# Performance work log

Measured on AMD Instinct MI355X. Metric: run time of the kernel, lower is better.

The kernel has to match this reference:

```python
import math
import jax, jax.numpy as jnp
import numpy as np

B, S, D, H = 4, 2048, 1024, 16
DH = D // H  # 64


def setup_inputs() -> dict:
    key = jax.random.key(0)
    k1, k2, k3 = jax.random.split(key, 3)
    x = jax.random.normal(k1, (B, S, D), dtype=jnp.float32)
    W_qkv = jax.random.normal(k2, (D, 3 * D), dtype=jnp.float32) * (1.0 / math.sqrt(D))
    b_qkv = jax.random.normal(k3, (3 * D,), dtype=jnp.float32) * 0.02
    return {"x": x, "W_qkv": W_qkv, "b_qkv": b_qkv}


def reference(x, W_qkv, b_qkv):
    b, s, d = x.shape
    qkv = x @ W_qkv + b_qkv                       # [B,S,3D]
    # Faithful to torch: view(B,S,H,3,D_h) -> interleaved per-head q/k/v split
    qkv = qkv.reshape(b, s, H, 3, DH)
    q = jnp.transpose(qkv[:, :, :, 0, :], (0, 2, 1, 3))  # [B,H,S,DH]
    k = jnp.transpose(qkv[:, :, :, 1, :], (0, 2, 1, 3))
    v = jnp.transpose(qkv[:, :, :, 2, :], (0, 2, 1, 3))
    scores = jnp.einsum('bhsd,bhtd->bhst', q, k) / math.sqrt(DH)  # [B,H,S,S]
    causal = jnp.triu(jnp.ones((s, s), dtype=bool), k=1)
    scores = jnp.where(causal, -jnp.inf, scores)
    weights = jax.nn.softmax(scores, axis=-1)
    # dropout is identity in eval/reference mode
    context = jnp.einsum('bhst,bhtd->bhsd', weights, v)  # [B,H,S,DH]
    return jnp.transpose(context, (0, 2, 1, 3)).reshape(b, s, d)
```

## Files before the change

### kernel.cpp

```cpp
#include <hip/hip_runtime.h>
#include <hip/hip_bf16.h>

#define Bz 4
#define Sz 2048
#define Dz 1024
#define Hz 16
#define DHz 64
#define Mz (Bz*Sz)
#define N3z (3*Dz)
#define Kz Dz

typedef short s16x8 __attribute__((ext_vector_type(8)));
typedef float f32x4 __attribute__((ext_vector_type(4)));
typedef unsigned short u16;

__device__ __forceinline__ u16 f2b(float f) {
  union { float f; unsigned u; } v; v.f = f;
  unsigned r = v.u + 0x7FFFu + ((v.u >> 16) & 1u);
  return (u16)(r >> 16);
}

__device__ __forceinline__ unsigned cvt_pk_bf16(float lo, float hi) {
  unsigned r;
  asm("v_cvt_pk_bf16_f32 %0, %1, %2" : "=v"(r) : "v"(lo), "v"(hi));
  return r;
}

__global__ __launch_bounds__(256) void cvt_x(const float* __restrict__ x,
                                             u16* __restrict__ xb) {
  int i = (blockIdx.x * 256 + threadIdx.x) * 4;
  float4 v = *reinterpret_cast<const float4*>(x + i);
  ushort4 o;
  o.x = f2b(v.x); o.y = f2b(v.y); o.z = f2b(v.z); o.w = f2b(v.w);
  *reinterpret_cast<ushort4*>(xb + i) = o;
}

__global__ __launch_bounds__(256) void transpose_w(const float* __restrict__ W,
                                                   u16* __restrict__ Wt) {
  __shared__ u16 t[32][33];
  int nb = blockIdx.x;
  int kb = blockIdx.y;
  int tx = threadIdx.x, ty = threadIdx.y;
#pragma unroll
  for (int j = 0; j < 4; ++j) {
    int k = kb * 32 + ty + j * 8;
    t[ty + j * 8][tx] = f2b(W[(size_t)k * N3z + nb * 32 + tx]);
  }
  __syncthreads();
#pragma unroll
  for (int j = 0; j < 4; ++j) {
    int n = nb * 32 + ty + j * 8;
    Wt[(size_t)n * Kz + kb * 32 + tx] = t[tx][ty + j * 8];
  }
}

#define BM 128
#define BN 128
#define BKs 32
#define QSCALE (0.125f * 1.44269504088896f)

__global__ __launch_bounds__(256) void qkv_gemm(
    const u16* __restrict__ A, const u16* __restrict__ Bt,
    const float* __restrict__ bias,
    u16* __restrict__ Qo, u16* __restrict__ Ko, u16* __restrict__ Vo) {
  __shared__ alignas(16) u16 As[BM * BKs];
  __shared__ alignas(16) u16 Bs[BN * BKs];
  const int tid = threadIdx.x;
  const int wid = tid >> 6, lane = tid & 63;
  const int wr = wid >> 1, wc = wid & 1;
  const int g = lane >> 4, lq = lane & 15;
  const int brow = blockIdx.x * BM;
  const int bcol = blockIdx.y * BN;

  f32x4 acc[4][4] = {};

  for (int kt = 0; kt < Kz; kt += BKs) {
#pragma unroll
    for (int c = 0; c < 2; ++c) {
      int row = (wid * 2 + c) * 16 + (lane >> 2);
      int off = (lane & 3) * 8;
      const u16* ga = A + (size_t)(brow + row) * Kz + kt + off;
      __builtin_amdgcn_global_load_lds(
          (const __attribute__((address_space(1))) void*)ga,
          (__attribute__((address_space(3))) void*)&As[(wid * 2 + c) * 512],
          16, 0, 0);
      const u16* gb = Bt + (size_t)(bcol + row) * Kz + kt + off;
      __builtin_amdgcn_global_load_lds(
          (const __attribute__((address_space(1))) void*)gb,
          (__attribute__((address_space(3))) void*)&Bs[(wid * 2 + c) * 512],
          16, 0, 0);
    }
    __syncthreads();

    s16x8 af[4], bfr[4];
#pragma unroll
    for (int i = 0; i < 4; ++i) {
      af[i]  = *reinterpret_cast<const s16x8*>(&As[(wr * 64 + i * 16 + lq) * BKs + g * 8]);
      bfr[i] = *reinterpret_cast<const s16x8*>(&Bs[(wc * 64 + i * 16 + lq) * BKs + g * 8]);
    }
#pragma unroll
    for (int mi = 0; mi < 4; ++mi)
#pragma unroll
      for (int ni = 0; ni < 4; ++ni)
        acc[mi][ni] = __builtin_amdgcn_mfma_f32_16x16x32_bf16(af[mi], bfr[ni], acc[mi][ni], 0, 0, 0);
    __syncthreads();
  }

#pragma unroll
  for (int ni = 0; ni < 4; ++ni) {
    int gcol = bcol + wc * 64 + ni * 16 + lq;
    int h = gcol / 192;
    int rem = gcol - h * 192;
    int tt = rem >> 6;
    int dh = rem & 63;
    float bv = bias[gcol];
    u16* dst = (tt == 0) ? Qo : (tt == 1) ? Ko : Vo;
    float scale = (tt == 0) ? QSCALE : 1.0f;
#pragma unroll
    for (int mi = 0; mi < 4; ++mi) {
#pragma unroll
      for (int r = 0; r < 4; ++r) {
        int grow = brow + wr * 64 + mi * 16 + g * 4 + r;
        int bb = grow >> 11;
        int ss = grow & 2047;
        float v = (acc[mi][ni][r] + bv) * scale;
        dst[(((size_t)bb * Hz + h) * Sz + ss) * DHz + dh] = f2b(v);
      }
    }
  }
}

__global__ __launch_bounds__(512, 4) void attn_kernel(
    const u16* __restrict__ Qg, const u16* __restrict__ Kg,
    const u16* __restrict__ Vg, float* __restrict__ out) {
  __shared__ alignas(16) u16 Ks[64 * 64];
  __shared__ alignas(16) u16 Vs[64 * 64];

  const int qpair = blockIdx.x;
  const int bh = blockIdx.y;
  const int tid = threadIdx.x;
  const int wid = tid >> 6, lane = tid & 63;
  const int g = lane >> 4, lq = lane & 15;
  const size_t base = (size_t)bh * Sz * DHz;
  const int b = bh >> 4, h = bh & 15;

  const int krow = tid >> 3;
  const int kslot = tid & 7;
  const int kswz = kslot ^ (krow & 7);
  const int vkey = tid & 63;
  const int vdh0 = (tid >> 6) * 8;

  char* KsB = (char*)Ks;
  char* VsB = (char*)Vs;

  const int p = g & 1;
  const int cb = g >> 1;
  const int sA = 32 * (g & 1) + lq;
  const int sB = sA + 16;
  const int sEven = cb ? sB : sA;
  const int sOdd  = cb ? sA : sB;

  for (int half = 0; half < 2; ++half) {
    const int qt = half ? (15 - qpair) : qpair;
    const int q0w = qt * 128 + wid * 16;
    const int qrow = q0w + lq;

    s16x8 qf0 = *reinterpret_cast<const s16x8*>(Qg + base + (size_t)(q0w + lq) * DHz + g * 8);
    s16x8 qf1 = *reinterpret_cast<const s16x8*>(Qg + base + (size_t)(q0w + lq) * DHz + g * 8 + 32);

    f32x4 o[4] = {};
    float m1 = -1e30f;
    float l1 = 0.f;

    const int nt = 2 * qt + 2;
    for (int t = 0; t < nt; ++t) {
      const int kv0 = t * 64;

      s16x8 kvv = *reinterpret_cast<const s16x8*>(Kg + base + (size_t)(kv0 + krow) * DHz + kslot * 8);
      *reinterpret_cast<s16x8*>(KsB + krow * 128 + kswz * 16) = kvv;
      s16x8 vvv = *reinterpret_cast<const s16x8*>(Vg + base + (size_t)(kv0 + vkey) * DHz + vdh0);
#pragma unroll
      for (int j = 0; j < 8; ++j) {
        int byte = (vdh0 + j) * 128 + vkey * 2;
        byte ^= (j << 4);
        *reinterpret_cast<u16*>(VsB + byte) = (u16)vvv[j];
      }
      __syncthreads();

      const bool active = (kv0 <= q0w + 15);
      if (active) {
        f32x4 z[4];
#pragma unroll
        for (int f = 0; f < 4; ++f) {
          int row = f * 16 + lq;
          s16x8 kb0 = *reinterpret_cast<const s16x8*>(KsB + row * 128 + ((g ^ (row & 7)) << 4));
          s16x8 kb1 = *reinterpret_cast<const s16x8*>(KsB + row * 128 + (((g + 4) ^ (row & 7)) << 4));
          f32x4 zz = {0.f, 0.f, 0.f, 0.f};
          zz = __builtin_amdgcn_mfma_f32_16x16x32_bf16(kb0, qf0, zz, 0, 0, 0);
          zz = __builtin_amdgcn_mfma_f32_16x16x32_bf16(kb1, qf1, zz, 0, 0, 0);
          z[f] = zz;
        }

        if (kv0 + 63 > q0w) {
#pragma unroll
          for (int f = 0; f < 4; ++f)
#pragma unroll
            for (int r = 0; r < 4; ++r) {
              int key = kv0 + f * 16 + g * 4 + r;
              if (key > qrow) z[f][r] = -1e30f;
            }
        }

        float pm = z[0][0];
#pragma unroll
        for (int f = 0; f < 4; ++f)
#pragma unroll
          for (int r = 0; r < 4; ++r) pm = fmaxf(pm, z[f][r]);
        pm = fmaxf(pm, __shfl_xor(pm, 16));
        pm = fmaxf(pm, __shfl_xor(pm, 32));

        if (!__all(pm <= m1 + 8.0f)) {
          float mn = fmaxf(m1, pm);
          float a = exp2f(m1 - mn);
          m1 = mn;
          l1 *= a;
          float a0 = __shfl(a, 4 * g + 0);
          float a1 = __shfl(a, 4 * g + 1);
          float a2 = __shfl(a, 4 * g + 2);
          float a3 = __shfl(a, 4 * g + 3);
#pragma unroll
          for (int ni = 0; ni < 4; ++ni) {
            o[ni][0] *= a0; o[ni][1] *= a1; o[ni][2] *= a2; o[ni][3] *= a3;
          }
        }

        float s = 0.f;
        unsigned w[4][2];
#pragma unroll
        for (int f = 0; f < 4; ++f) {
          float p0 = exp2f(z[f][0] - m1);
          float p1 = exp2f(z[f][1] - m1);
          float p2 = exp2f(z[f][2] - m1);
          float p3 = exp2f(z[f][3] - m1);
          s += (p0 + p1) + (p2 + p3);
          w[f][0] = cvt_pk_bf16(p0, p1);
          w[f][1] = cvt_pk_bf16(p2, p3);
        }
        s += __shfl_xor(s, 16);
        s += __shfl_xor(s, 32);
        l1 += s;

        int e0 = __shfl((int)(p ? w[1][0] : w[0][0]), sEven);
        int o0 = __shfl((int)(p ? w[0][0] : w[1][0]), sOdd);
        int e1 = __shfl((int)(p ? w[1][1] : w[0][1]), sEven);
        int o1 = __shfl((int)(p ? w[0][1] : w[1][1]), sOdd);
        int e2 = __shfl((int)(p ? w[3][0] : w[2][0]), sEven);
        int o2 = __shfl((int)(p ? w[2][0] : w[3][0]), sOdd);
        int e3 = __shfl((int)(p ? w[3][1] : w[2][1]), sEven);
        int o3 = __shfl((int)(p ? w[2][1] : w[3][1]), sOdd);
        union { int i[4]; s16x8 v; } A0, A1;
        A0.i[0] = cb ? o0 : e0;
        A0.i[2] = cb ? e0 : o0;
        A0.i[1] = cb ? o1 : e1;
        A0.i[3] = cb ? e1 : o1;
        A1.i[0] = cb ? o2 : e2;
        A1.i[2] = cb ? e2 : o2;
        A1.i[1] = cb ? o3 : e3;
        A1.i[3] = cb ? e3 : o3;

#pragma unroll
        for (int ni = 0; ni < 4; ++ni) {
          int row = ni * 16 + lq;
          s16x8 vb0 = *reinterpret_cast<const s16x8*>(VsB + row * 128 + ((g ^ (row & 7)) << 4));
          s16x8 vb1 = *reinterpret_cast<const s16x8*>(VsB + row * 128 + (((g + 4) ^ (row & 7)) << 4));
          o[ni] = __builtin_amdgcn_mfma_f32_16x16x32_bf16(A0.v, vb0, o[ni], 0, 0, 0);
          o[ni] = __builtin_amdgcn_mfma_f32_16x16x32_bf16(A1.v, vb1, o[ni], 0, 0, 0);
        }
      }
      __syncthreads();
    }

    float lr0 = __shfl(l1, 4 * g + 0);
    float lr1 = __shfl(l1, 4 * g + 1);
    float lr2 = __shfl(l1, 4 * g + 2);
    float lr3 = __shfl(l1, 4 * g + 3);
    float inv[4] = {1.0f / lr0, 1.0f / lr1, 1.0f / lr2, 1.0f / lr3};
#pragma unroll
    for (int r = 0; r < 4; ++r) {
      int s = q0w + g * 4 + r;
      float* op = out + (((size_t)b * Sz + s) * Hz + h) * DHz;
#pragma unroll
      for (int ni = 0; ni < 4; ++ni)
        op[ni * 16 + lq] = o[ni][r] * inv[r];
    }
  }
}

extern "C" void kernel_launch(void* const* d_in, const int* in_sizes, int n_in,
                              void* d_out, int out_size, void* d_ws, size_t ws_size,
                              hipStream_t stream) {
  const float* x    = (const float*)d_in[0];
  const float* W    = (const float*)d_in[1];
  const float* bias = (const float*)d_in[2];
  float* out = (float*)d_out;

  char* ws = (char*)d_ws;
  u16* xb = (u16*)(ws);
  u16* wt = (u16*)(ws + 16777216);
  u16* Qb = (u16*)(ws + 23068672);
  u16* Kb = (u16*)(ws + 39845888);
  u16* Vb = (u16*)(ws + 56623104);

  cvt_x<<<8192, 256, 0, stream>>>(x, xb);
  transpose_w<<<dim3(96, 32), dim3(32, 8), 0, stream>>>(W, wt);
  qkv_gemm<<<dim3(Mz / BM, N3z / BN), 256, 0, stream>>>(xb, wt, bias, Qb, Kb, Vb);
  attn_kernel<<<dim3(8, Bz * Hz), 512, 0, stream>>>(Qb, Kb, Vb, out);
}
```

Before: 233.5 us.

## Double-buffer K/V tiles in attention and widen GEMM K-tile with swizzled LDS

The attention kernel now keeps two LDS buffers for K and V. It prefetches the next tile into registers while the current one is being computed, then writes it to the other buffer, which removes one barrier per iteration and hides global load latency. The QKV GEMM moves to a 64-wide K tile with an XOR-swizzled LDS layout, halving the number of loop iterations and barriers and avoiding bank conflicts on fragment reads. In exchange, LDS use and register pressure go up, which may cut occupancy.

```diff
diff --git a/kernel.cpp b/kernel.cpp
--- a/kernel.cpp
+++ b/kernel.cpp
@@ -56,7 +56,7 @@
 
 #define BM 128
 #define BN 128
-#define BKs 32
+#define BKs 64
 #define QSCALE (0.125f * 1.44269504088896f)
 
 __global__ __launch_bounds__(256) void qkv_gemm(
@@ -72,37 +72,44 @@
   const int brow = blockIdx.x * BM;
   const int bcol = blockIdx.y * BN;
 
+  const int soff = (((lane & 7) ^ (lane >> 3))) * 8;
+
   f32x4 acc[4][4] = {};
 
   for (int kt = 0; kt < Kz; kt += BKs) {
 #pragma unroll
-    for (int c = 0; c < 2; ++c) {
-      int row = (wid * 2 + c) * 16 + (lane >> 2);
-      int off = (lane & 3) * 8;
-      const u16* ga = A + (size_t)(brow + row) * Kz + kt + off;
+    for (int c = 0; c < 4; ++c) {
+      int row = (wid * 4 + c) * 8 + (lane >> 3);
+      const u16* ga = A + (size_t)(brow + row) * Kz + kt + soff;
       __builtin_amdgcn_global_load_lds(
           (const __attribute__((address_space(1))) void*)ga,
-          (__attribute__((address_space(3))) void*)&As[(wid * 2 + c) * 512],
+          (__attribute__((address_space(3))) void*)&As[(wid * 4 + c) * 512],
           16, 0, 0);
-      const u16* gb = Bt + (size_t)(bcol + row) * Kz + kt + off;
+      const u16* gb = Bt + (size_t)(bcol + row) * Kz + kt + soff;
       __builtin_amdgcn_global_load_lds(
           (const __attribute__((address_space(1))) void*)gb,
-          (__attribute__((address_space(3))) void*)&Bs[(wid * 2 + c) * 512],
+          (__attribute__((address_space(3))) void*)&Bs[(wid * 4 + c) * 512],
           16, 0, 0);
     }
     __syncthreads();
 
-    s16x8 af[4], bfr[4];
-#pragma unroll
-    for (int i = 0; i < 4; ++i) {
-      af[i]  = *reinterpret_cast<const s16x8*>(&As[(wr * 64 + i * 16 + lq) * BKs + g * 8]);
-      bfr[i] = *reinterpret_cast<const s16x8*>(&Bs[(wc * 64 + i * 16 + lq) * BKs + g * 8]);
-    }
-#pragma unroll
-    for (int mi = 0; mi < 4; ++mi)
-#pragma unroll
-      for (int ni = 0; ni < 4; ++ni)
-        acc[mi][ni] = __builtin_amdgcn_mfma_f32_16x16x32_bf16(af[mi], bfr[ni], acc[mi][ni], 0, 0, 0);
+#pragma unroll
+    for (int ks = 0; ks < 2; ++ks) {
+      s16x8 af[4], bfr[4];
+#pragma unroll
+      for (int i = 0; i < 4; ++i) {
+        int rowa = wr * 64 + i * 16 + lq;
+        int rowb = wc * 64 + i * 16 + lq;
+        int sl = ((ks * 4 + g) ^ (lq & 7)) << 4;
+        af[i]  = *reinterpret_cast<const s16x8*>((const char*)As + rowa * 128 + sl);
+        bfr[i] = *reinterpret_cast<const s16x8*>((const char*)Bs + rowb * 128 + sl);
+      }
+#pragma unroll
+      for (int mi = 0; mi < 4; ++mi)
+#pragma unroll
+        for (int ni = 0; ni < 4; ++ni)
+          acc[mi][ni] = __builtin_amdgcn_mfma_f32_16x16x32_bf16(af[mi], bfr[ni], acc[mi][ni], 0, 0, 0);
+    }
     __syncthreads();
   }
 
@@ -133,8 +140,8 @@
 __global__ __launch_bounds__(512, 4) void attn_kernel(
     const u16* __restrict__ Qg, const u16* __restrict__ Kg,
     const u16* __restrict__ Vg, float* __restrict__ out) {
-  __shared__ alignas(16) u16 Ks[64 * 64];
-  __shared__ alignas(16) u16 Vs[64 * 64];
+  __shared__ alignas(16) u16 Ks[2][64 * 64];
+  __shared__ alignas(16) u16 Vs[2][64 * 64];
 
   const int qpair = blockIdx.x;
   const int bh = blockIdx.y;
@@ -150,9 +157,6 @@
   const int vkey = tid & 63;
   const int vdh0 = (tid >> 6) * 8;
 
-  char* KsB = (char*)Ks;
-  char* VsB = (char*)Vs;
-
   const int p = g & 1;
   const int cb = g >> 1;
   const int sA = 32 * (g & 1) + lq;
@@ -173,19 +177,33 @@
     float l1 = 0.f;
 
     const int nt = 2 * qt + 2;
+
+    {
+      s16x8 kc = *reinterpret_cast<const s16x8*>(Kg + base + (size_t)krow * DHz + kslot * 8);
+      s16x8 vc = *reinterpret_cast<const s16x8*>(Vg + base + (size_t)vkey * DHz + vdh0);
+      char* KB = (char*)Ks[0];
+      char* VB = (char*)Vs[0];
+      *reinterpret_cast<s16x8*>(KB + krow * 128 + kswz * 16) = kc;
+#pragma unroll
+      for (int j = 0; j < 8; ++j)
+        *reinterpret_cast<u16*>(VB + (((vdh0 + j) * 128 + vkey * 2) ^ (j << 4))) = (u16)vc[j];
+    }
+    __syncthreads();
+
+    int cur = 0;
     for (int t = 0; t < nt; ++t) {
       const int kv0 = t * 64;
-
-      s16x8 kvv = *reinterpret_cast<const s16x8*>(Kg + base + (size_t)(kv0 + krow) * DHz + kslot * 8);
-      *reinterpret_cast<s16x8*>(KsB + krow * 128 + kswz * 16) = kvv;
-      s16x8 vvv = *reinterpret_cast<const s16x8*>(Vg + base + (size_t)(kv0 + vkey) * DHz + vdh0);
-#pragma unroll
-      for (int j = 0; j < 8; ++j) {
-        int byte = (vdh0 + j) * 128 + vkey * 2;
-        byte ^= (j << 4);
-        *reinterpret_cast<u16*>(VsB + byte) = (u16)vvv[j];
-      }
-      __syncthreads();
+      const bool more = (t + 1 < nt);
+
+      s16x8 kn, vn;
+      if (more) {
+        const int nv0 = kv0 + 64;
+        kn = *reinterpret_cast<const s16x8*>(Kg + base + (size_t)(nv0 + krow) * DHz + kslot * 8);
+        vn = *reinterpret_cast<const s16x8*>(Vg + base + (size_t)(nv0 + vkey) * DHz + vdh0);
+      }
+
+      const char* KsC = (const char*)Ks[0] + cur * 8192;
+      const char* VsC = (const char*)Vs[0] + cur * 8192;
 
       const bool active = (kv0 <= q0w + 15);
       if (active) {
@@ -193,8 +211,8 @@
 #pragma unroll
         for (int f = 0; f < 4; ++f) {
           int row = f * 16 + lq;
-          s16x8 kb0 = *reinterpret_cast<const s16x8*>(KsB + row * 128 + ((g ^ (row & 7)) << 4));
-          s16x8 kb1 = *reinterpret_cast<const s16x8*>(KsB + row * 128 + (((g + 4) ^ (row & 7)) << 4));
+          s16x8 kb0 = *reinterpret_cast<const s16x8*>(KsC + row * 128 + ((g ^ (row & 7)) << 4));
+          s16x8 kb1 = *reinterpret_cast<const s16x8*>(KsC + row * 128 + (((g + 4) ^ (row & 7)) << 4));
           f32x4 zz = {0.f, 0.f, 0.f, 0.f};
           zz = __builtin_amdgcn_mfma_f32_16x16x32_bf16(kb0, qf0, zz, 0, 0, 0);
           zz = __builtin_amdgcn_mfma_f32_16x16x32_bf16(kb1, qf1, zz, 0, 0, 0);
@@ -271,13 +289,23 @@
 #pragma unroll
         for (int ni = 0; ni < 4; ++ni) {
           int row = ni * 16 + lq;
-          s16x8 vb0 = *reinterpret_cast<const s16x8*>(VsB + row * 128 + ((g ^ (row & 7)) << 4));
-          s16x8 vb1 = *reinterpret_cast<const s16x8*>(VsB + row * 128 + (((g + 4) ^ (row & 7)) << 4));
+          s16x8 vb0 = *reinterpret_cast<const s16x8*>(VsC + row * 128 + ((g ^ (row & 7)) << 4));
+          s16x8 vb1 = *reinterpret_cast<const s16x8*>(VsC + row * 128 + (((g + 4) ^ (row & 7)) << 4));
           o[ni] = __builtin_amdgcn_mfma_f32_16x16x32_bf16(A0.v, vb0, o[ni], 0, 0, 0);
           o[ni] = __builtin_amdgcn_mfma_f32_16x16x32_bf16(A1.v, vb1, o[ni], 0, 0, 0);
         }
       }
+
+      if (more) {
+        char* KB = (char*)Ks[0] + (cur ^ 1) * 8192;
+        char* VB = (char*)Vs[0] + (cur ^ 1) * 8192;
+        *reinterpret_cast<s16x8*>(KB + krow * 128 + kswz * 16) = kn;
+#pragma unroll
+        for (int j = 0; j < 8; ++j)
+          *reinterpret_cast<u16*>(VB + (((vdh0 + j) * 128 + vkey * 2) ^ (j << 4))) = (u16)vn[j];
+      }
       __syncthreads();
+      cur ^= 1;
     }
 
     float lr0 = __shfl(l1, 4 * g + 0);
```

New measurement: 238.5 us. 2.2% more time.
